# Optimization experiments

Hardware: AMD Instinct MI355X
Metric: run time of the kernel (lower is better)

Reference implementation:

```python
import jax, jax.numpy as jnp
import numpy as np

N_TOKENS = 16384
DIM = 2048
N_EXPERTS = 64
TOPK = 8
ROUTE_SCALE = 1.0


def setup_inputs() -> dict:
    key = jax.random.key(0)
    k1, k2 = jax.random.split(key)
    x = jax.random.normal(k1, (N_TOKENS, DIM), dtype=jnp.float32)
    W = jax.random.normal(k2, (N_EXPERTS, DIM), dtype=jnp.float32) * 0.02
    return {"x": x, "W": W}


def reference(x, W):
    # linear scores: [tokens, n_experts]
    logits = jnp.einsum('td,ed->te', x, W)
    # softmax in float32 (score_func == 'softmax'); bias is None since dim != 64
    scores = jax.nn.softmax(logits.astype(jnp.float32), axis=-1)
    # top-k expert selection, then gather original scores at selected indices
    _, indices = jax.lax.top_k(scores, TOPK)
    weights = jnp.take_along_axis(scores, indices, axis=-1)
    # softmax path: no renormalization, just route scaling
    weights = (weights * ROUTE_SCALE).astype(x.dtype)
    return weights, indices
```

## Files before the change

### kernel.cpp

```cpp
#include <hip/hip_runtime.h>


typedef __attribute__((ext_vector_type(8))) short short8;
typedef __attribute__((ext_vector_type(16))) float f32x16;
typedef __attribute__((ext_vector_type(4))) float f32x4;
typedef __attribute__((ext_vector_type(4))) unsigned int u32x4;

#define NT    16384
#define DIMK  2048
#define NE    64
#define TOPKK 8
#define TT    32
#define WS_BYTES (32 * 24 * 1024)

union U4S8 { unsigned int u[4]; short8 s; u32x4 v; };

__device__ __forceinline__ short8 as_s8(u32x4 v) { U4S8 t; t.v = v; return t.s; }

__device__ __forceinline__ void split3(const float4 a, const float4 b,
                                       short8& H, short8& M, short8& L) {
    const float f[8] = {a.x, a.y, a.z, a.w, b.x, b.y, b.z, b.w};
    U4S8 uh, um, ul;
#pragma unroll
    for (int p = 0; p < 4; ++p) {
        const float f0 = f[2 * p], f1 = f[2 * p + 1];
        const unsigned int t0 = __float_as_uint(f0) & 0xFFFF0000u;
        const unsigned int t1 = __float_as_uint(f1) & 0xFFFF0000u;
        uh.u[p] = (t0 >> 16) | t1;
        const float r0 = f0 - __uint_as_float(t0);
        const float r1 = f1 - __uint_as_float(t1);
        const unsigned int v0 = __float_as_uint(r0) & 0xFFFF0000u;
        const unsigned int v1 = __float_as_uint(r1) & 0xFFFF0000u;
        um.u[p] = (v0 >> 16) | v1;
        const float s0 = r0 - __uint_as_float(v0);
        const float s1 = r1 - __uint_as_float(v1);
        ul.u[p] = (__float_as_uint(s0) >> 16) | (__float_as_uint(s1) & 0xFFFF0000u);
    }
    H = uh.s; M = um.s; L = ul.s;
}

__device__ __forceinline__ f32x16 mfma6w(short8 ah, short8 am, short8 al,
                                         short8 bh, short8 bm, short8 bl,
                                         f32x16 c) {
    c = __builtin_amdgcn_mfma_f32_32x32x16_bf16(ah, bh, c, 0, 0, 0);
    c = __builtin_amdgcn_mfma_f32_32x32x16_bf16(ah, bm, c, 0, 0, 0);
    c = __builtin_amdgcn_mfma_f32_32x32x16_bf16(am, bh, c, 0, 0, 0);
    c = __builtin_amdgcn_mfma_f32_32x32x16_bf16(ah, bl, c, 0, 0, 0);
    c = __builtin_amdgcn_mfma_f32_32x32x16_bf16(am, bm, c, 0, 0, 0);
    c = __builtin_amdgcn_mfma_f32_32x32x16_bf16(al, bh, c, 0, 0, 0);
    return c;
}

__global__ __launch_bounds__(64) void pack_w_kernel(
    const float* __restrict__ W, short* __restrict__ wpk)
{
    const int b  = blockIdx.x;
    const int c  = b >> 3, fg = b & 7;
    const int s  = fg >> 1, n32 = fg & 1;
    const int l  = threadIdx.x;
    const float* g = W + (size_t)(32 * n32 + (l & 31)) * DIMK
                       + 64 * c + 16 * s + 8 * (l >> 5);
    const float4 lo = *(const float4*)g;
    const float4 hi = *(const float4*)(g + 4);
    short8 H, M, L;
    split3(lo, hi, H, M, L);
    const size_t base = ((size_t)(c * 8 + fg) * 3) * 512 + l * 8;
    *(short8*)(wpk + base)        = H;
    *(short8*)(wpk + base + 512)  = M;
    *(short8*)(wpk + base + 1024) = L;
}

#define XLOADP(d0, d1, p)                                                     \
    asm volatile("global_load_dwordx4 %0, %2, off\n\t"                        \
                 "global_load_dwordx4 %1, %2, off offset:16"                  \
                 : "=&v"(d0), "=&v"(d1) : "v"(p))
#define WLOAD3(d0, d1, d2, p)                                                 \
    asm volatile("global_load_dwordx4 %0, %3, off\n\t"                        \
                 "global_load_dwordx4 %1, %3, off offset:1024\n\t"            \
                 "global_load_dwordx4 %2, %3, off offset:2048"                \
                 : "=&v"(d0), "=&v"(d1), "=&v"(d2) : "v"(p))
#define WAITN(n) do {                                                         \
    asm volatile("s_waitcnt vmcnt(" #n ")");                                  \
    __builtin_amdgcn_sched_barrier(0);                                        \
} while (0)

__global__ __launch_bounds__(512, 2) void gate_main_kernel(
    const float* __restrict__ x, const short* __restrict__ wpk,
    float* __restrict__ out)
{
    __shared__ float lg[8][TT][NE + 1];

    const int tid = threadIdx.x;
    const int w   = tid >> 6;
    const int l   = tid & 63;
    const int r31 = l & 31;
    const int l5  = l >> 5;
    const int bt0 = blockIdx.x * TT;

    const float* xp = x + (size_t)(bt0 + r31) * DIMK + w * 256 + l5 * 8;
    const short* wq0 = wpk + (size_t)w * 49152 + l * 8;
    const short* wq1 = wq0 + 1536;

    f32x16 acc0, acc1;
#pragma unroll
    for (int i = 0; i < 16; ++i) { acc0[i] = 0.f; acc1[i] = 0.f; }

    float4 xv[4][2];
    u32x4  w0v[2][3], w1v[2][3];

    XLOADP(xv[0][0], xv[0][1], xp); xp += 16;
    XLOADP(xv[1][0], xv[1][1], xp); xp += 16;
    XLOADP(xv[2][0], xv[2][1], xp); xp += 16;
    WLOAD3(w0v[0][0], w0v[0][1], w0v[0][2], wq0); wq0 += 3072;
    WLOAD3(w1v[0][0], w1v[0][1], w1v[0][2], wq1); wq1 += 3072;

#pragma unroll
    for (int j = 0; j < 16; ++j) {
        const int jb = j & 3;
        const int jn = (j + 1) & 1;
        const int jc = j & 1;
        if (j <= 12) {
            XLOADP(xv[(j + 3) & 3][0], xv[(j + 3) & 3][1], xp); xp += 16;
        }
        if (j <= 14) {
            WLOAD3(w0v[jn][0], w0v[jn][1], w0v[jn][2], wq0); wq0 += 3072;
        }
        if (j <= 12)      WAITN(8);
        else if (j <= 14) WAITN(6);
        else              WAITN(3);

        short8 H, M, L;
        split3(xv[jb][0], xv[jb][1], H, M, L);
        acc0 = mfma6w(H, M, L, as_s8(w0v[jc][0]), as_s8(w0v[jc][1]),
                      as_s8(w0v[jc][2]), acc0);

        if (j <= 14) {
            WLOAD3(w1v[jn][0], w1v[jn][1], w1v[jn][2], wq1); wq1 += 3072;
        }
        if (j <= 12)      WAITN(8);
        else if (j <= 14) WAITN(6);
        else              WAITN(0);

        acc1 = mfma6w(H, M, L, as_s8(w1v[jc][0]), as_s8(w1v[jc][1]),
                      as_s8(w1v[jc][2]), acc1);
    }

#pragma unroll
    for (int r = 0; r < 16; ++r) {
        const int rowc = (r & 3) + 8 * (r >> 2) + 4 * l5;
        lg[w][rowc][r31]      = acc0[r];
        lg[w][rowc][32 + r31] = acc1[r];
    }
    __syncthreads();

#pragma unroll
    for (int rr = 0; rr < (TT * NE) / 512; ++rr) {
        const int idx = tid + rr * 512;
        const int t = idx >> 6, e = idx & 63;
        lg[0][t][e] = ((lg[0][t][e] + lg[1][t][e]) + (lg[2][t][e] + lg[3][t][e]))
                    + ((lg[4][t][e] + lg[5][t][e]) + (lg[6][t][e] + lg[7][t][e]));
    }
    __syncthreads();

    if (tid < TT) {
        const float* rowp = &lg[0][tid][0];
        float mx = -3.402823466e38f;
        for (int e = 0; e < NE; ++e) mx = fmaxf(mx, rowp[e]);
        float sden = 0.f;
        for (int e = 0; e < NE; ++e) sden += expf(rowp[e] - mx);

        float tv[TOPKK];
        int   ti[TOPKK];
#pragma unroll
        for (int i = 0; i < TOPKK; ++i) { tv[i] = -3.402823466e38f; ti[i] = 0; }
        for (int e = 0; e < NE; ++e) {
            const float v = rowp[e];
            if (v > tv[TOPKK - 1]) {
                tv[TOPKK - 1] = v; ti[TOPKK - 1] = e;
#pragma unroll
                for (int q = TOPKK - 1; q > 0; --q) {
                    if (tv[q] > tv[q - 1]) {
                        const float fv = tv[q]; tv[q] = tv[q - 1]; tv[q - 1] = fv;
                        const int   iv = ti[q]; ti[q] = ti[q - 1]; ti[q - 1] = iv;
                    }
                }
            }
        }
        float* ow = out + (size_t)(bt0 + tid) * TOPKK;
        float* oi = out + (size_t)NT * TOPKK + (size_t)(bt0 + tid) * TOPKK;
#pragma unroll
        for (int i = 0; i < TOPKK; ++i) {
            ow[i] = expf(tv[i] - mx) / sden;
            oi[i] = (float)ti[i];
        }
    }
}

__device__ __forceinline__ f32x4 mfma6s(short8 ah, short8 am, short8 al,
                                        short8 bh, short8 bm, short8 bl, f32x4 c) {
    c = __builtin_amdgcn_mfma_f32_16x16x32_bf16(ah, bh, c, 0, 0, 0);
    c = __builtin_amdgcn_mfma_f32_16x16x32_bf16(ah, bm, c, 0, 0, 0);
    c = __builtin_amdgcn_mfma_f32_16x16x32_bf16(am, bh, c, 0, 0, 0);
    c = __builtin_amdgcn_mfma_f32_16x16x32_bf16(ah, bl, c, 0, 0, 0);
    c = __builtin_amdgcn_mfma_f32_16x16x32_bf16(am, bm, c, 0, 0, 0);
    c = __builtin_amdgcn_mfma_f32_16x16x32_bf16(al, bh, c, 0, 0, 0);
    return c;
}

__device__ __forceinline__ void load_step(const float* xp0, const float* xp1,
                                          const float* wp, int koff,
                                          float4 xb[2][2], float4 wb[4][2]) {
#pragma unroll
    for (int h = 0; h < 2; ++h) {
        xb[0][h] = *(const float4*)(xp0 + koff + 4 * h);
        xb[1][h] = *(const float4*)(xp1 + koff + 4 * h);
    }
#pragma unroll
    for (int n = 0; n < 4; ++n)
#pragma unroll
        for (int h = 0; h < 2; ++h)
            wb[n][h] = *(const float4*)(wp + (size_t)n * 16 * DIMK + koff + 4 * h);
}

__device__ __forceinline__ void do_step(const float4 xc[2][2], const float4 wc[4][2],
                                        f32x4 acc[2][4]) {
    short8 ah[2], am[2], al[2];
#pragma unroll
    for (int m = 0; m < 2; ++m) split3(xc[m][0], xc[m][1], ah[m], am[m], al[m]);
#pragma unroll
    for (int n = 0; n < 4; ++n) {
        short8 bh, bm, bl;
        split3(wc[n][0], wc[n][1], bh, bm, bl);
#pragma unroll
        for (int m = 0; m < 2; ++m)
            acc[m][n] = mfma6s(ah[m], am[m], al[m], bh, bm, bl, acc[m][n]);
    }
}

__global__ __launch_bounds__(256, 2) void gate_fallback_kernel(
    const float* __restrict__ x, const float* __restrict__ W,
    float* __restrict__ out)
{
    __shared__ float lg[4][32][NE + 1];
    const int tid = threadIdx.x;
    const int w = tid >> 6, l = tid & 63;
    const int j = l & 15, g = l >> 4;
    const int bt0 = blockIdx.x * 32;
    const int kb = w * 512;
    const float* xp0 = x + (size_t)(bt0 + j) * DIMK + kb + 8 * g;
    const float* xp1 = xp0 + (size_t)16 * DIMK;
    const float* wpp = W + (size_t)j * DIMK + kb + 8 * g;
    f32x4 acc[2][4];
#pragma unroll
    for (int m = 0; m < 2; ++m)
#pragma unroll
        for (int n = 0; n < 4; ++n) acc[m][n] = (f32x4){0.f, 0.f, 0.f, 0.f};
    float4 xA[2][2], wA[4][2], xB[2][2], wB[4][2];
    load_step(xp0, xp1, wpp, 0, xA, wA);
#pragma unroll 1
    for (int s = 0; s < 16; s += 2) {
        load_step(xp0, xp1, wpp, 32 * (s + 1), xB, wB);
        do_step(xA, wA, acc);
        if (s + 2 < 16) load_step(xp0, xp1, wpp, 32 * (s + 2), xA, wA);
        do_step(xB, wB, acc);
    }
#pragma unroll
    for (int m = 0; m < 2; ++m)
#pragma unroll
        for (int n = 0; n < 4; ++n)
#pragma unroll
            for (int q = 0; q < 4; ++q)
                lg[w][16 * m + 4 * g + q][16 * n + j] = acc[m][n][q];
    __syncthreads();
#pragma unroll
    for (int r = 0; r < 8; ++r) {
        const int idx = tid + r * 256;
        const int t = idx >> 6, e = idx & 63;
        lg[0][t][e] += lg[1][t][e] + lg[2][t][e] + lg[3][t][e];
    }
    __syncthreads();
    if (tid < 32) {
        const float* rowp = &lg[0][tid][0];
        float mx = -3.402823466e38f;
        for (int e = 0; e < NE; ++e) mx = fmaxf(mx, rowp[e]);
        float sden = 0.f;
        for (int e = 0; e < NE; ++e) sden += expf(rowp[e] - mx);
        float tv[TOPKK]; int ti[TOPKK];
#pragma unroll
        for (int i = 0; i < TOPKK; ++i) { tv[i] = -3.402823466e38f; ti[i] = 0; }
        for (int e = 0; e < NE; ++e) {
            const float v = rowp[e];
            if (v > tv[TOPKK - 1]) {
                tv[TOPKK - 1] = v; ti[TOPKK - 1] = e;
#pragma unroll
                for (int q = TOPKK - 1; q > 0; --q)
                    if (tv[q] > tv[q - 1]) {
                        const float fv = tv[q]; tv[q] = tv[q - 1]; tv[q - 1] = fv;
                        const int iv = ti[q]; ti[q] = ti[q - 1]; ti[q - 1] = iv;
                    }
            }
        }
        float* ow = out + (size_t)(bt0 + tid) * TOPKK;
        float* oi = out + (size_t)NT * TOPKK + (size_t)(bt0 + tid) * TOPKK;
#pragma unroll
        for (int i = 0; i < TOPKK; ++i) {
            ow[i] = expf(tv[i] - mx) / sden;
            oi[i] = (float)ti[i];
        }
    }
}

extern "C" void kernel_launch(void* const* d_in, const int* in_sizes, int n_in,
                              void* d_out, int out_size, void* d_ws, size_t ws_size,
                              hipStream_t stream) {
    const float* x = (const float*)d_in[0];
    const float* W = (const float*)d_in[1];
    float* out = (float*)d_out;
    if (ws_size >= (size_t)WS_BYTES) {
        short* wpk = (short*)d_ws;
        hipLaunchKernelGGL(pack_w_kernel, dim3(256), dim3(64), 0, stream, W, wpk);
        hipLaunchKernelGGL(gate_main_kernel, dim3(NT / TT), dim3(512), 0, stream,
                           x, wpk, out);
    } else {
        hipLaunchKernelGGL(gate_fallback_kernel, dim3(NT / 32), dim3(256), 0, stream,
                           x, W, out);
    }
}
```

Measured before the change: 62.37 us.

## Stage x tiles into LDS via async global_load_lds and double token tile

Doubles the per-block token tile to 64 and splits the 8 waves into 2 token halves by 4 K-quarters. Each wave streams its x rows into a swizzled 3-stage LDS ring with async global-to-LDS loads, and keeps a deeper 4-stage register pipeline for the pre-split weights. This halves the number of blocks that re-read the packed W, cuts the cross-wave reduction from 8 partials to 4, and moves x loads off VGPRs. In exchange occupancy drops to one block per CU, each wave runs a longer K loop, and correctness depends on the hand-tuned vmcnt wait counts.

```diff
diff --git a/kernel.cpp b/kernel.cpp
--- a/kernel.cpp
+++ b/kernel.cpp
@@ -10,7 +10,7 @@
 #define DIMK  2048
 #define NE    64
 #define TOPKK 8
-#define TT    32
+#define TT    64
 #define WS_BYTES (32 * 24 * 1024)
 
 union U4S8 { unsigned int u[4]; short8 s; u32x4 v; };
@@ -70,86 +70,119 @@
     *(short8*)(wpk + base + 1024) = L;
 }
 
-#define XLOADP(d0, d1, p)                                                     \
-    asm volatile("global_load_dwordx4 %0, %2, off\n\t"                        \
-                 "global_load_dwordx4 %1, %2, off offset:16"                  \
-                 : "=&v"(d0), "=&v"(d1) : "v"(p))
 #define WLOAD3(d0, d1, d2, p)                                                 \
     asm volatile("global_load_dwordx4 %0, %3, off\n\t"                        \
                  "global_load_dwordx4 %1, %3, off offset:1024\n\t"            \
                  "global_load_dwordx4 %2, %3, off offset:2048"                \
                  : "=&v"(d0), "=&v"(d1), "=&v"(d2) : "v"(p))
 #define WAITN(n) do {                                                         \
-    asm volatile("s_waitcnt vmcnt(" #n ")");                                  \
+    asm volatile("s_waitcnt vmcnt(" #n ")" ::: "memory");                     \
     __builtin_amdgcn_sched_barrier(0);                                        \
 } while (0)
 
-__global__ __launch_bounds__(512, 2) void gate_main_kernel(
+__device__ __forceinline__ void async16(void* lds, const void* gp) {
+    __builtin_amdgcn_global_load_lds(
+        (const __attribute__((address_space(1))) unsigned int*)gp,
+        (__attribute__((address_space(3))) unsigned int*)lds, 16, 0, 0);
+}
+
+__global__ __launch_bounds__(512, 1) void gate_main_kernel(
     const float* __restrict__ x, const short* __restrict__ wpk,
     float* __restrict__ out)
 {
-    __shared__ float lg[8][TT][NE + 1];
+    __shared__ __align__(16) char smem[8 * 3 * 4096];
 
     const int tid = threadIdx.x;
     const int w   = tid >> 6;
     const int l   = tid & 63;
     const int r31 = l & 31;
     const int l5  = l >> 5;
+    const int tw  = w & 1;
+    const int kq  = w >> 2 >= 0 ? (w >> 1) : 0;
     const int bt0 = blockIdx.x * TT;
 
-    const float* xp = x + (size_t)(bt0 + r31) * DIMK + w * 256 + l5 * 8;
-    const short* wq0 = wpk + (size_t)w * 49152 + l * 8;
+    char* wbase = smem + w * 12288;
+    const int swr = (r31 & 7) ^ (((r31 >> 3) & 3) << 1);
+
+    const int srow = l >> 3;
+    const int sg0  = (l & 7) ^ srow;
+    const float* xrow0 = x + (size_t)(bt0 + 32 * tw + srow) * DIMK + kq * 512;
+
+#define STAGE_CHUNK(k) do {                                                   \
+    _Pragma("unroll")                                                         \
+    for (int i = 0; i < 4; ++i) {                                             \
+        const float* gsrc = xrow0 + (size_t)(8 * i) * DIMK + (k) * 32         \
+                          + ((sg0 ^ (2 * i)) << 2);                           \
+        async16(wbase + ((k) % 3) * 4096 + i * 1024, gsrc);                   \
+    }                                                                         \
+} while (0)
+
+    const short* wq0 = wpk + (size_t)kq * 98304 + l * 8;
     const short* wq1 = wq0 + 1536;
 
     f32x16 acc0, acc1;
 #pragma unroll
     for (int i = 0; i < 16; ++i) { acc0[i] = 0.f; acc1[i] = 0.f; }
 
-    float4 xv[4][2];
-    u32x4  w0v[2][3], w1v[2][3];
-
-    XLOADP(xv[0][0], xv[0][1], xp); xp += 16;
-    XLOADP(xv[1][0], xv[1][1], xp); xp += 16;
-    XLOADP(xv[2][0], xv[2][1], xp); xp += 16;
+    u32x4 w0v[4][3], w1v[4][3];
+
+    STAGE_CHUNK(0);
+    STAGE_CHUNK(1);
+    STAGE_CHUNK(2);
     WLOAD3(w0v[0][0], w0v[0][1], w0v[0][2], wq0); wq0 += 3072;
     WLOAD3(w1v[0][0], w1v[0][1], w1v[0][2], wq1); wq1 += 3072;
-
-#pragma unroll
-    for (int j = 0; j < 16; ++j) {
-        const int jb = j & 3;
-        const int jn = (j + 1) & 1;
-        const int jc = j & 1;
-        if (j <= 12) {
-            XLOADP(xv[(j + 3) & 3][0], xv[(j + 3) & 3][1], xp); xp += 16;
-        }
-        if (j <= 14) {
-            WLOAD3(w0v[jn][0], w0v[jn][1], w0v[jn][2], wq0); wq0 += 3072;
-        }
-        if (j <= 12)      WAITN(8);
-        else if (j <= 14) WAITN(6);
-        else              WAITN(3);
-
-        short8 H, M, L;
-        split3(xv[jb][0], xv[jb][1], H, M, L);
-        acc0 = mfma6w(H, M, L, as_s8(w0v[jc][0]), as_s8(w0v[jc][1]),
-                      as_s8(w0v[jc][2]), acc0);
-
-        if (j <= 14) {
-            WLOAD3(w1v[jn][0], w1v[jn][1], w1v[jn][2], wq1); wq1 += 3072;
-        }
-        if (j <= 12)      WAITN(8);
-        else if (j <= 14) WAITN(6);
-        else              WAITN(0);
-
-        acc1 = mfma6w(H, M, L, as_s8(w1v[jc][0]), as_s8(w1v[jc][1]),
-                      as_s8(w1v[jc][2]), acc1);
-    }
-
+    WLOAD3(w0v[1][0], w0v[1][1], w0v[1][2], wq0); wq0 += 3072;
+    WLOAD3(w1v[1][0], w1v[1][1], w1v[1][2], wq1); wq1 += 3072;
+    WLOAD3(w0v[2][0], w0v[2][1], w0v[2][2], wq0); wq0 += 3072;
+    WLOAD3(w1v[2][0], w1v[2][1], w1v[2][2], wq1); wq1 += 3072;
+
+#define SLICE(t) do {                                                         \
+    if ((t) <= 28) {                                                          \
+        WLOAD3(w0v[((t)+3)&3][0], w0v[((t)+3)&3][1], w0v[((t)+3)&3][2], wq0); \
+        wq0 += 3072;                                                          \
+        WLOAD3(w1v[((t)+3)&3][0], w1v[((t)+3)&3][1], w1v[((t)+3)&3][2], wq1); \
+        wq1 += 3072;                                                          \
+    }                                                                         \
+    if ((t) <= 1)            WAITN(18);                                       \
+    else if ((t) == 29)      WAITN(12);                                       \
+    else if ((t) == 30)      WAITN(6);                                        \
+    else if ((t) == 31)      WAITN(0);                                        \
+    else if (((t) & 1) || (t) == 2 || (t) == 28) WAITN(22);                   \
+    else                     WAITN(26);                                       \
+    {                                                                         \
+        const char* xb = wbase + (((t) >> 1) % 3) * 4096;                     \
+        const float4 a0 = *(const float4*)(xb + r31 * 128 +                   \
+            (((((t) & 1) * 4 + 2 * l5 + 0) ^ swr) << 4));                     \
+        const float4 a1 = *(const float4*)(xb + r31 * 128 +                   \
+            (((((t) & 1) * 4 + 2 * l5 + 1) ^ swr) << 4));                     \
+        short8 H, M, L;                                                       \
+        split3(a0, a1, H, M, L);                                              \
+        acc0 = mfma6w(H, M, L, as_s8(w0v[(t)&3][0]), as_s8(w0v[(t)&3][1]),    \
+                      as_s8(w0v[(t)&3][2]), acc0);                            \
+        acc1 = mfma6w(H, M, L, as_s8(w1v[(t)&3][0]), as_s8(w1v[(t)&3][1]),    \
+                      as_s8(w1v[(t)&3][2]), acc1);                            \
+    }                                                                         \
+    if (((t) & 1) && (t) <= 25) STAGE_CHUNK(((t) + 5) >> 1);                  \
+} while (0)
+
+    SLICE(0);  SLICE(1);  SLICE(2);  SLICE(3);
+    SLICE(4);  SLICE(5);  SLICE(6);  SLICE(7);
+    SLICE(8);  SLICE(9);  SLICE(10); SLICE(11);
+    SLICE(12); SLICE(13); SLICE(14); SLICE(15);
+    SLICE(16); SLICE(17); SLICE(18); SLICE(19);
+    SLICE(20); SLICE(21); SLICE(22); SLICE(23);
+    SLICE(24); SLICE(25); SLICE(26); SLICE(27);
+    SLICE(28); SLICE(29); SLICE(30); SLICE(31);
+
+    __syncthreads();
+
+    float* lg = (float*)smem;
 #pragma unroll
     for (int r = 0; r < 16; ++r) {
         const int rowc = (r & 3) + 8 * (r >> 2) + 4 * l5;
-        lg[w][rowc][r31]      = acc0[r];
-        lg[w][rowc][32 + r31] = acc1[r];
+        const int trow = 32 * tw + rowc;
+        lg[(kq * TT + trow) * (NE + 1) + r31]      = acc0[r];
+        lg[(kq * TT + trow) * (NE + 1) + 32 + r31] = acc1[r];
     }
     __syncthreads();
 
@@ -157,13 +190,14 @@
     for (int rr = 0; rr < (TT * NE) / 512; ++rr) {
         const int idx = tid + rr * 512;
         const int t = idx >> 6, e = idx & 63;
-        lg[0][t][e] = ((lg[0][t][e] + lg[1][t][e]) + (lg[2][t][e] + lg[3][t][e]))
-                    + ((lg[4][t][e] + lg[5][t][e]) + (lg[6][t][e] + lg[7][t][e]));
+        lg[t * (NE + 1) + e] =
+            (lg[t * (NE + 1) + e] + lg[(TT + t) * (NE + 1) + e]) +
+            (lg[(2 * TT + t) * (NE + 1) + e] + lg[(3 * TT + t) * (NE + 1) + e]);
     }
     __syncthreads();
 
     if (tid < TT) {
-        const float* rowp = &lg[0][tid][0];
+        const float* rowp = lg + tid * (NE + 1);
         float mx = -3.402823466e38f;
         for (int e = 0; e < NE; ++e) mx = fmaxf(mx, rowp[e]);
         float sden = 0.f;
@@ -194,6 +228,8 @@
             oi[i] = (float)ti[i];
         }
     }
+#undef SLICE
+#undef STAGE_CHUNK
 }
 
 __device__ __forceinline__ f32x4 mfma6s(short8 ah, short8 am, short8 al,
```

Result: faster. 51.64 us (-17.2%).
